# Kernel optimization log

Hardware: AMD Instinct MI355X
Metric: run time of the kernel (lower is better)

## Reference

```python
import jax, jax.numpy as jnp
import numpy as np

RES_DIM = 8192
BATCH = 128
DENSITY = 0.02
NNZ = int(DENSITY * RES_DIM * RES_DIM)  # 1342177
LEAK = 0.6
BIAS = 1.6


def setup_inputs() -> dict:
    key = jax.random.key(0)
    k1, k2, k3, k4, k5 = jax.random.split(key, 5)
    proj_vars = jax.random.normal(k1, (BATCH, RES_DIM), dtype=jnp.float32)
    res_state = jax.random.normal(k2, (BATCH, RES_DIM), dtype=jnp.float32)
    # COO representation of the sparse reservoir matrix wr (what BCOO stores).
    # Values scaled so the effective spectral radius is O(spec_rad), keeping
    # tanh out of full saturation (init-time normalization detail).
    scale = 0.8 / np.sqrt(DENSITY * RES_DIM)
    wr_vals = jax.random.normal(k3, (NNZ,), dtype=jnp.float32) * scale
    wr_rows = jnp.sort(jax.random.randint(k4, (NNZ,), 0, RES_DIM, dtype=jnp.int32))
    wr_cols = jax.random.randint(k5, (NNZ,), 0, RES_DIM, dtype=jnp.int32)
    return {
        "proj_vars": proj_vars,
        "res_state": res_state,
        "wr_vals": wr_vals,
        "wr_rows": wr_rows,
        "wr_cols": wr_cols,
    }


def reference(proj_vars, res_state, wr_vals, wr_rows, wr_cols):
    # Batched sparse matvec: y[b, i] = sum_k vals[k] * res_state[b, cols[k]] for rows[k]==i
    # gather -> [nnz, batch], scale by vals, scatter-add over rows (sorted).
    contrib = wr_vals[:, None] * res_state.T[wr_cols]           # [nnz, B]
    y = jax.ops.segment_sum(contrib, wr_rows, num_segments=RES_DIM,
                            indices_are_sorted=True)            # [res_dim, B]
    res_next = jnp.tanh(y.T + proj_vars + BIAS)                  # [B, res_dim]
    return LEAK * res_next + (1.0 - LEAK) * res_state
```

## Files before the change

### kernel.cpp

```cpp
#include <hip/hip_runtime.h>
#include <hip/hip_bf16.h>
#include <stdint.h>

#define RES_DIM 8192
#define BATCH   128
#define NNZ     1342177
#define LEAK    0.6f
#define BIAS    1.6f

#define CONV_BLOCKS 1024
#define BND_THREADS ((NNZ + 3) / 4)
#define BND_BLOCKS  ((BND_THREADS + 255) / 256)

__device__ __forceinline__ float fast_tanh(float x) {
    float e = __expf(2.0f * x);
    return 1.0f - 2.0f / (e + 1.0f);
}

__device__ __forceinline__ uint32_t f32_to_bf16_rne(float f) {
    uint32_t u = __float_as_uint(f);
    return (u + 0x7fffu + ((u >> 16) & 1u)) >> 16;
}

__global__ __launch_bounds__(256) void prep_kernel(
    const float* __restrict__ in, uint32_t* __restrict__ st2,
    const int* __restrict__ rows, int* __restrict__ row_start) {
    if (blockIdx.x < CONV_BLOCKS) {
        __shared__ float tile[32][33];
        const int bx = blockIdx.x & 255;
        const int by = blockIdx.x >> 8;
        const int tx = threadIdx.x & 31, ty = threadIdx.x >> 5;
        const int r0 = bx * 32, b0 = by * 32;
#pragma unroll
        for (int j = 0; j < 32; j += 8)
            tile[ty + j][tx] = in[(size_t)(b0 + ty + j) * RES_DIM + r0 + tx];
        __syncthreads();
#pragma unroll
        for (int i = threadIdx.x; i < 512; i += 256) {
            int rl = i >> 4, pl = i & 15;
            uint32_t lo = f32_to_bf16_rne(tile[2 * pl + 0][rl]);
            uint32_t hi = f32_to_bf16_rne(tile[2 * pl + 1][rl]);
            st2[(size_t)(r0 + rl) * 64 + (b0 >> 1) + pl] = lo | (hi << 16);
        }
    } else {
        const int t  = (blockIdx.x - CONV_BLOCKS) * 256 + threadIdx.x;
        const int k4 = t * 4;
        if (k4 >= NNZ) return;
        if (k4 + 4 <= NNZ) {
            const int4 R = *(const int4*)(rows + k4);
            if (k4 == 0)
                for (int r = 0; r <= R.x; ++r) row_start[r] = 0;
            const int rn = rows[k4 + 4];
            for (int r = R.x + 1; r <= R.y; ++r) row_start[r] = k4 + 1;
            for (int r = R.y + 1; r <= R.z; ++r) row_start[r] = k4 + 2;
            for (int r = R.z + 1; r <= R.w; ++r) row_start[r] = k4 + 3;
            for (int r = R.w + 1; r <= rn;  ++r) row_start[r] = k4 + 4;
        } else {
            const int r1 = rows[k4];
            for (int r = r1 + 1; r <= RES_DIM; ++r) row_start[r] = NNZ;
        }
    }
}

#define FMA8(G, v)                                              \
    do {                                                        \
        a0 = fmaf(v, __uint_as_float((G).x << 16), a0);         \
        a1 = fmaf(v, __uint_as_float((G).x & 0xffff0000u), a1); \
        a2 = fmaf(v, __uint_as_float((G).y << 16), a2);         \
        a3 = fmaf(v, __uint_as_float((G).y & 0xffff0000u), a3); \
        a4 = fmaf(v, __uint_as_float((G).z << 16), a4);         \
        a5 = fmaf(v, __uint_as_float((G).z & 0xffff0000u), a5); \
        a6 = fmaf(v, __uint_as_float((G).w << 16), a6);         \
        a7 = fmaf(v, __uint_as_float((G).w & 0xffff0000u), a7); \
    } while (0)

template <int BF16Y>
__global__ __launch_bounds__(256, 8) void spmm_kernel(
    const float* __restrict__ vals, const int* __restrict__ cols,
    const int* __restrict__ row_start, const uint32_t* __restrict__ st2,
    void* __restrict__ yT) {
    const int t = threadIdx.x;
    const int w = t >> 6;
    const int l = t & 63;
    const int g = l >> 4;
    const int j = l & 15;
    const int r = (blockIdx.x & 7) * (RES_DIM / 8) + (blockIdx.x >> 3);

    const int ks = row_start[r];
    const int ke = row_start[r + 1];
    const int ka = min(ke, (ks + 3) & ~3);
    const int U  = (ke - ka) >> 4;
    const int ts = ka + (U << 4);

    const uint32_t* tp = st2 + j * 4;
    float a0 = 0, a1 = 0, a2 = 0, a3 = 0, a4 = 0, a5 = 0, a6 = 0, a7 = 0;

    if (w == 0 && ks < ka) {
        const int kk = ks + g;
        int c = 0; float v = 0.0f;
        if (kk < ka) { c = cols[kk]; v = vals[kk]; }
        const uint4 G = *(const uint4*)(tp + (size_t)c * 64);
        FMA8(G, v);
    }
    if (w == 1 && ts < ke) {
#pragma unroll
        for (int i = 0; i < 4; ++i) {
            const int kk = ts + 4 * i + g;
            int c = 0; float v = 0.0f;
            if (kk < ke) { c = cols[kk]; v = vals[kk]; }
            const uint4 G = *(const uint4*)(tp + (size_t)c * 64);
            FMA8(G, v);
        }
    }
    for (int u = w; u < U; u += 4) {
        const int base = ka + (u << 4) + 4 * g;
        const int4   C = *(const int4*)(cols + base);
        const float4 V = *(const float4*)(vals + base);
        const uint4 G0 = *(const uint4*)(tp + (size_t)C.x * 64);
        const uint4 G1 = *(const uint4*)(tp + (size_t)C.y * 64);
        const uint4 G2 = *(const uint4*)(tp + (size_t)C.z * 64);
        const uint4 G3 = *(const uint4*)(tp + (size_t)C.w * 64);
        FMA8(G0, V.x);
        FMA8(G1, V.y);
        FMA8(G2, V.z);
        FMA8(G3, V.w);
    }

    a0 += __shfl_xor(a0, 16, 64); a0 += __shfl_xor(a0, 32, 64);
    a1 += __shfl_xor(a1, 16, 64); a1 += __shfl_xor(a1, 32, 64);
    a2 += __shfl_xor(a2, 16, 64); a2 += __shfl_xor(a2, 32, 64);
    a3 += __shfl_xor(a3, 16, 64); a3 += __shfl_xor(a3, 32, 64);
    a4 += __shfl_xor(a4, 16, 64); a4 += __shfl_xor(a4, 32, 64);
    a5 += __shfl_xor(a5, 16, 64); a5 += __shfl_xor(a5, 32, 64);
    a6 += __shfl_xor(a6, 16, 64); a6 += __shfl_xor(a6, 32, 64);
    a7 += __shfl_xor(a7, 16, 64); a7 += __shfl_xor(a7, 32, 64);

    __shared__ float red[4][16][8];
    if (l < 16) {
        *(float4*)&red[w][j][0] = make_float4(a0, a1, a2, a3);
        *(float4*)&red[w][j][4] = make_float4(a4, a5, a6, a7);
    }
    __syncthreads();
    if (t < BATCH) {
        const int jj = t >> 3, ii = t & 7;
        float s = red[0][jj][ii] + red[1][jj][ii] + red[2][jj][ii] + red[3][jj][ii];
        if (BF16Y) {
            float shi = __shfl_down(s, 1, 64);
            if (!(t & 1))
                ((uint32_t*)yT)[(size_t)r * 64 + (t >> 1)] =
                    f32_to_bf16_rne(s) | (f32_to_bf16_rne(shi) << 16);
        } else {
            ((float*)yT)[(size_t)r * BATCH + t] = s;
        }
    }
}

template <int BF16Y>
__global__ __launch_bounds__(256) void epi_kernel(
    const void* __restrict__ yT, const float* __restrict__ proj,
    const float* __restrict__ res, float* __restrict__ out) {
    __shared__ float tile[64][33];
    const int r0 = blockIdx.x * 64;
    const int b0 = blockIdx.y * 32;
    const int t  = threadIdx.x;
#pragma unroll
    for (int p = 0; p < 2; ++p) {
        const int rl = p * 32 + (t >> 3);
        const int bq = (t & 7) * 4;
        float x, y, z, wv;
        if (BF16Y) {
            ushort4 u = *(const ushort4*)((const uint16_t*)yT +
                         (size_t)(r0 + rl) * BATCH + b0 + bq);
            x  = __uint_as_float((uint32_t)u.x << 16);
            y  = __uint_as_float((uint32_t)u.y << 16);
            z  = __uint_as_float((uint32_t)u.z << 16);
            wv = __uint_as_float((uint32_t)u.w << 16);
        } else {
            float4 v = *(const float4*)((const float*)yT +
                         (size_t)(r0 + rl) * BATCH + b0 + bq);
            x = v.x; y = v.y; z = v.z; wv = v.w;
        }
        tile[rl][bq + 0] = x; tile[rl][bq + 1] = y;
        tile[rl][bq + 2] = z; tile[rl][bq + 3] = wv;
    }
    __syncthreads();
#pragma unroll
    for (int p = 0; p < 2; ++p) {
        const int bl = p * 16 + (t >> 4);
        const int rq = (t & 15) * 4;
        const size_t oi = (size_t)(b0 + bl) * RES_DIM + r0 + rq;
        const float4 pj = *(const float4*)(proj + oi);
        const float4 rs = *(const float4*)(res + oi);
        float4 o;
        o.x = LEAK * fast_tanh(tile[rq + 0][bl] + pj.x + BIAS) + (1.0f - LEAK) * rs.x;
        o.y = LEAK * fast_tanh(tile[rq + 1][bl] + pj.y + BIAS) + (1.0f - LEAK) * rs.y;
        o.z = LEAK * fast_tanh(tile[rq + 2][bl] + pj.z + BIAS) + (1.0f - LEAK) * rs.z;
        o.w = LEAK * fast_tanh(tile[rq + 3][bl] + pj.w + BIAS) + (1.0f - LEAK) * rs.w;
        *(float4*)(out + oi) = o;
    }
}

extern "C" void kernel_launch(void* const* d_in, const int* in_sizes, int n_in,
                              void* d_out, int out_size, void* d_ws, size_t ws_size,
                              hipStream_t stream) {
    const float* proj      = (const float*)d_in[0];
    const float* res_state = (const float*)d_in[1];
    const float* wr_vals   = (const float*)d_in[2];
    const int*   wr_rows   = (const int*)d_in[3];
    const int*   wr_cols   = (const int*)d_in[4];
    float*       out       = (float*)d_out;

    uint8_t*  ws        = (uint8_t*)d_ws;
    uint32_t* st2       = (uint32_t*)ws;
    int*      row_start = (int*)(ws + 2097152);
    uint8_t*  yT        = ws + 2130176;
    const bool f32y = ws_size >= (2130176ull + (size_t)RES_DIM * BATCH * 4);

    prep_kernel<<<CONV_BLOCKS + BND_BLOCKS, 256, 0, stream>>>(
        res_state, st2, wr_rows, row_start);

    if (f32y) {
        spmm_kernel<0><<<RES_DIM, 256, 0, stream>>>(wr_vals, wr_cols, row_start, st2, yT);
        epi_kernel<0><<<dim3(RES_DIM / 64, BATCH / 32), 256, 0, stream>>>(yT, proj, res_state, out);
    } else {
        spmm_kernel<1><<<RES_DIM, 256, 0, stream>>>(wr_vals, wr_cols, row_start, st2, yT);
        epi_kernel<1><<<dim3(RES_DIM / 64, BATCH / 32), 256, 0, stream>>>(yT, proj, res_state, out);
    }
}
```

Measured before the change: 35.79 us.

## Process two rows per block with software-pipelined gathers in SpMM

Each 256-thread block now handles two sparse rows, with two wavefronts per row instead of four, halving the grid size. The main loop is software-pipelined so the next chunk's column, value and gathered state loads are issued before the current chunk's FMAs. Gather addressing switches to 32-bit byte offsets. The aim is to hide gather latency and cut per-block overhead, at the cost of more registers (launch bounds lowered to 4 blocks) and less parallelism per row.

```diff
diff --git a/kernel.cpp b/kernel.cpp
--- a/kernel.cpp
+++ b/kernel.cpp
@@ -75,16 +75,19 @@
     } while (0)
 
 template <int BF16Y>
-__global__ __launch_bounds__(256, 8) void spmm_kernel(
+__global__ __launch_bounds__(256, 4) void spmm_kernel(
     const float* __restrict__ vals, const int* __restrict__ cols,
     const int* __restrict__ row_start, const uint32_t* __restrict__ st2,
     void* __restrict__ yT) {
-    const int t = threadIdx.x;
-    const int w = t >> 6;
-    const int l = t & 63;
-    const int g = l >> 4;
-    const int j = l & 15;
-    const int r = (blockIdx.x & 7) * (RES_DIM / 8) + (blockIdx.x >> 3);
+    const int t  = threadIdx.x;
+    const int w  = t >> 6;
+    const int rw = w >> 1;
+    const int wr = w & 1;
+    const int l  = t & 63;
+    const int g  = l >> 4;
+    const int j  = l & 15;
+    const int bp = (blockIdx.x & 7) * (RES_DIM / 16) + (blockIdx.x >> 3);
+    const int r  = bp * 2 + rw;
 
     const int ks = row_start[r];
     const int ke = row_start[r + 1];
@@ -92,38 +95,57 @@
     const int U  = (ke - ka) >> 4;
     const int ts = ka + (U << 4);
 
-    const uint32_t* tp = st2 + j * 4;
+    const char* stb = (const char*)st2;
+    const uint32_t joff = (uint32_t)j << 4;
     float a0 = 0, a1 = 0, a2 = 0, a3 = 0, a4 = 0, a5 = 0, a6 = 0, a7 = 0;
 
-    if (w == 0 && ks < ka) {
+    if (wr == 0 && ks < ka) {
         const int kk = ks + g;
         int c = 0; float v = 0.0f;
         if (kk < ka) { c = cols[kk]; v = vals[kk]; }
-        const uint4 G = *(const uint4*)(tp + (size_t)c * 64);
+        const uint4 G = *(const uint4*)(stb + (((uint32_t)c << 8) + joff));
         FMA8(G, v);
     }
-    if (w == 1 && ts < ke) {
+    if (wr == 1 && ts < ke) {
 #pragma unroll
         for (int i = 0; i < 4; ++i) {
             const int kk = ts + 4 * i + g;
             int c = 0; float v = 0.0f;
             if (kk < ke) { c = cols[kk]; v = vals[kk]; }
-            const uint4 G = *(const uint4*)(tp + (size_t)c * 64);
+            const uint4 G = *(const uint4*)(stb + (((uint32_t)c << 8) + joff));
             FMA8(G, v);
         }
     }
-    for (int u = w; u < U; u += 4) {
+
+    int u = wr;
+    int4 C; float4 V; uint4 G0, G1, G2, G3;
+    if (u < U) {
         const int base = ka + (u << 4) + 4 * g;
-        const int4   C = *(const int4*)(cols + base);
-        const float4 V = *(const float4*)(vals + base);
-        const uint4 G0 = *(const uint4*)(tp + (size_t)C.x * 64);
-        const uint4 G1 = *(const uint4*)(tp + (size_t)C.y * 64);
-        const uint4 G2 = *(const uint4*)(tp + (size_t)C.z * 64);
-        const uint4 G3 = *(const uint4*)(tp + (size_t)C.w * 64);
+        C = *(const int4*)(cols + base);
+        V = *(const float4*)(vals + base);
+        G0 = *(const uint4*)(stb + (((uint32_t)C.x << 8) + joff));
+        G1 = *(const uint4*)(stb + (((uint32_t)C.y << 8) + joff));
+        G2 = *(const uint4*)(stb + (((uint32_t)C.z << 8) + joff));
+        G3 = *(const uint4*)(stb + (((uint32_t)C.w << 8) + joff));
+    }
+    while (u < U) {
+        const int un = u + 2;
+        int4 Cn; float4 Vn; uint4 H0, H1, H2, H3;
+        if (un < U) {
+            const int base = ka + (un << 4) + 4 * g;
+            Cn = *(const int4*)(cols + base);
+            Vn = *(const float4*)(vals + base);
+            H0 = *(const uint4*)(stb + (((uint32_t)Cn.x << 8) + joff));
+            H1 = *(const uint4*)(stb + (((uint32_t)Cn.y << 8) + joff));
+            H2 = *(const uint4*)(stb + (((uint32_t)Cn.z << 8) + joff));
+            H3 = *(const uint4*)(stb + (((uint32_t)Cn.w << 8) + joff));
+        }
         FMA8(G0, V.x);
         FMA8(G1, V.y);
         FMA8(G2, V.z);
         FMA8(G3, V.w);
+        u = un;
+        C = Cn; V = Vn; G0 = H0; G1 = H1; G2 = H2; G3 = H3;
     }
 
     a0 += __shfl_xor(a0, 16, 64); a0 += __shfl_xor(a0, 32, 64);
@@ -135,22 +157,25 @@
     a6 += __shfl_xor(a6, 16, 64); a6 += __shfl_xor(a6, 32, 64);
     a7 += __shfl_xor(a7, 16, 64); a7 += __shfl_xor(a7, 32, 64);
 
-    __shared__ float red[4][16][8];
+    __shared__ float red[2][2][16][8];
     if (l < 16) {
-        *(float4*)&red[w][j][0] = make_float4(a0, a1, a2, a3);
-        *(float4*)&red[w][j][4] = make_float4(a4, a5, a6, a7);
+        *(float4*)&red[rw][wr][j][0] = make_float4(a0, a1, a2, a3);
+        *(float4*)&red[rw][wr][j][4] = make_float4(a4, a5, a6, a7);
     }
     __syncthreads();
-    if (t < BATCH) {
-        const int jj = t >> 3, ii = t & 7;
-        float s = red[0][jj][ii] + red[1][jj][ii] + red[2][jj][ii] + red[3][jj][ii];
+    {
+        const int rowsel = t >> 7;
+        const int b  = t & 127;
+        const int jj = b >> 3, ii = b & 7;
+        const int ro = bp * 2 + rowsel;
+        float s = red[rowsel][0][jj][ii] + red[rowsel][1][jj][ii];
         if (BF16Y) {
             float shi = __shfl_down(s, 1, 64);
-            if (!(t & 1))
-                ((uint32_t*)yT)[(size_t)r * 64 + (t >> 1)] =
+            if (!(b & 1))
+                ((uint32_t*)yT)[(size_t)ro * 64 + (b >> 1)] =
                     f32_to_bf16_rne(s) | (f32_to_bf16_rne(shi) << 16);
         } else {
-            ((float*)yT)[(size_t)r * BATCH + t] = s;
+            ((float*)yT)[(size_t)ro * BATCH + b] = s;
         }
     }
 }
@@ -220,10 +245,10 @@
         res_state, st2, wr_rows, row_start);
 
     if (f32y) {
-        spmm_kernel<0><<<RES_DIM, 256, 0, stream>>>(wr_vals, wr_cols, row_start, st2, yT);
+        spmm_kernel<0><<<RES_DIM / 2, 256, 0, stream>>>(wr_vals, wr_cols, row_start, st2, yT);
         epi_kernel<0><<<dim3(RES_DIM / 64, BATCH / 32), 256, 0, stream>>>(yT, proj, res_state, out);
     } else {
-        spmm_kernel<1><<<RES_DIM, 256, 0, stream>>>(wr_vals, wr_cols, row_start, st2, yT);
+        spmm_kernel<1><<<RES_DIM / 2, 256, 0, stream>>>(wr_vals, wr_cols, row_start, st2, yT);
         epi_kernel<1><<<dim3(RES_DIM / 64, BATCH / 32), 256, 0, stream>>>(yT, proj, res_state, out);
     }
 }
```

Result: no change. 35.52 us (-0.8%).
